# Kernel optimization log

Hardware: AMD Instinct MI355X
Metric: run time of the kernel (lower is better)

The kernel has to match this reference:

```python
import jax, jax.numpy as jnp
import numpy as np

NUM_ATOMS = 100000
NUM_BONDS = 200000
MAX_NB = 6
ATOM_FDIM = 133
BOND_FDIM = 147
HIDDEN = 300
DEPTH = 4
NUM_MOLS = 8192


def setup_inputs() -> dict:
    key = jax.random.key(0)
    ks = jax.random.split(key, 10)
    f_atoms = jax.random.normal(ks[0], (NUM_ATOMS, ATOM_FDIM), dtype=jnp.float32)
    f_bonds = jax.random.normal(ks[1], (NUM_BONDS, BOND_FDIM), dtype=jnp.float32)
    a2b = jax.random.randint(ks[2], (NUM_ATOMS, MAX_NB), 0, NUM_BONDS, dtype=jnp.int32)
    b2a = jax.random.randint(ks[3], (NUM_BONDS,), 0, NUM_ATOMS, dtype=jnp.int32)
    b2revb = jax.random.randint(ks[4], (NUM_BONDS,), 0, NUM_BONDS, dtype=jnp.int32)
    mol_ids = jnp.sort(jax.random.randint(ks[5], (NUM_ATOMS,), 0, NUM_MOLS, dtype=jnp.int32))
    s = 1.0 / np.sqrt(HIDDEN)
    W_i = jax.random.uniform(ks[6], (BOND_FDIM, HIDDEN), jnp.float32, -s, s)
    W_h = jax.random.uniform(ks[7], (HIDDEN, HIDDEN), jnp.float32, -s, s)
    W_o = jax.random.uniform(ks[8], (ATOM_FDIM + HIDDEN, HIDDEN), jnp.float32, -s, s)
    b_o = jax.random.uniform(ks[9], (HIDDEN,), jnp.float32, -s, s)
    return {"f_atoms": f_atoms, "f_bonds": f_bonds, "W_i": W_i, "W_h": W_h,
            "W_o": W_o, "b_o": b_o, "a2b": a2b, "b2a": b2a, "b2revb": b2revb,
            "mol_ids": mol_ids}


def reference(f_atoms, f_bonds, W_i, W_h, W_o, b_o, a2b, b2a, b2revb, mol_ids):
    # initial bond messages: W_i then activation (bias=False)
    inp = f_bonds @ W_i                       # [B, H]
    message = jax.nn.relu(inp)
    for _ in range(DEPTH - 1):
        nei = message[a2b]                    # [A, MAX_NB, H] gather
        a_message = nei.sum(axis=1)           # [A, H]
        rev_message = message[b2revb]         # [B, H]
        message = a_message[b2a] - rev_message
        message = jax.nn.relu(inp + message @ W_h)
    # final atom readout
    a_message = message[a2b].sum(axis=1)      # [A, H]
    a_input = jnp.concatenate([f_atoms, a_message], axis=1)
    atom_hiddens = jax.nn.relu(a_input @ W_o + b_o)
    # per-molecule mean aggregation (== chemprop a_scope loop with 'mean')
    sums = jax.ops.segment_sum(atom_hiddens, mol_ids, num_segments=NUM_MOLS)
    counts = jax.ops.segment_sum(jnp.ones((NUM_ATOMS,), jnp.float32), mol_ids,
                                 num_segments=NUM_MOLS)
    return sums / jnp.maximum(counts, 1.0)[:, None]
```

## Files before the change

### kernel.cpp

```cpp
#include <hip/hip_runtime.h>


#define DEVFN static __device__ __forceinline__

typedef __attribute__((ext_vector_type(8))) __bf16 bf16x8;
typedef __attribute__((ext_vector_type(4))) float floatx4;

DEVFN unsigned short f2bf(float f) {
    unsigned int u = __float_as_uint(f);
    u += 0x7FFFu + ((u >> 16) & 1u);
    return (unsigned short)(u >> 16);
}
DEVFN float bf2f(unsigned int u) { return __uint_as_float(u << 16); }

DEVFN unsigned int bfsub2(unsigned int a, unsigned int m) {
    float lo = bf2f(a & 0xffffu) - bf2f(m & 0xffffu);
    float hi = bf2f(a >> 16) - bf2f(m >> 16);
    return (unsigned int)f2bf(lo) | ((unsigned int)f2bf(hi) << 16);
}
DEVFN uint4 bfsub8(uint4 a, uint4 m) {
    return make_uint4(bfsub2(a.x, m.x), bfsub2(a.y, m.y),
                      bfsub2(a.z, m.z), bfsub2(a.w, m.w));
}

__global__ __launch_bounds__(256) void dbg_fill(float* out, int n, float v) {
    int t = blockIdx.x * 256 + threadIdx.x;
    if (t < n) out[t] = v;
}

__global__ __launch_bounds__(256) void prep_wih(const float* __restrict__ Wi,
                                                const float* __restrict__ Wh,
                                                unsigned short* __restrict__ Wt) {
    int t = blockIdx.x * 256 + threadIdx.x;
    if (t >= 320 * 480) return;
    int n = t / 480, k = t - n * 480;
    float v = 0.f;
    if (n < 300) {
        if (k < 147) v = Wi[k * 300 + n];
        else if (k >= 160 && k < 460) v = Wh[(k - 160) * 300 + n];
    }
    Wt[t] = f2bf(v);
}

__global__ __launch_bounds__(256) void prep_wto(const float* __restrict__ Wo,
                                                unsigned short* __restrict__ Wt) {
    int t = blockIdx.x * 256 + threadIdx.x;
    if (t >= 320 * 448) return;
    int n = t / 448, k = t - n * 448;
    float v = 0.f;
    if (n < 300) {
        if (k < 300) v = Wo[(133 + k) * 300 + n];
        else if (k >= 304 && k < 437) v = Wo[(k - 304) * 300 + n];
    }
    Wt[t] = f2bf(v);
}

__global__ __launch_bounds__(256) void pad_bonds(const float* __restrict__ fb,
                                                 unsigned short* __restrict__ out) {
    int t = blockIdx.x * 256 + threadIdx.x;
    if (t >= 200000 * 20) return;
    int b = t / 20, c = t - b * 20;
    unsigned int o[4];
#pragma unroll
    for (int p = 0; p < 4; ++p) {
        int sc = c * 8 + p * 2;
        float v0 = (sc < 147) ? fb[(size_t)b * 147 + sc] : 0.f;
        float v1 = (sc + 1 < 147) ? fb[(size_t)b * 147 + sc + 1] : 0.f;
        o[p] = (unsigned int)f2bf(v0) | ((unsigned int)f2bf(v1) << 16);
    }
    *(uint4*)(out + (size_t)b * 160 + c * 8) = make_uint4(o[0], o[1], o[2], o[3]);
}

__global__ __launch_bounds__(256) void atoms_concat(const float* __restrict__ fa,
                                                    unsigned short* __restrict__ concat) {
    int t = blockIdx.x * 256 + threadIdx.x;
    if (t >= 100000 * 18) return;
    int a = t / 18, c = t - a * 18;
    unsigned int o[4];
#pragma unroll
    for (int p = 0; p < 4; ++p) {
        int sc = c * 8 + p * 2;
        float v0 = (sc < 133) ? fa[(size_t)a * 133 + sc] : 0.f;
        float v1 = (sc + 1 < 133) ? fa[(size_t)a * 133 + sc + 1] : 0.f;
        o[p] = (unsigned int)f2bf(v0) | ((unsigned int)f2bf(v1) << 16);
    }
    *(uint4*)(concat + (size_t)a * 448 + 304 + c * 8) = make_uint4(o[0], o[1], o[2], o[3]);
}

template <int CH>
__global__ __launch_bounds__(256) void gather_sum(const unsigned short* __restrict__ msg,
                                                  const int* __restrict__ a2b,
                                                  unsigned short* __restrict__ out,
                                                  int ostride, int nA) {
    int t = blockIdx.x * 256 + threadIdx.x;
    if (t >= nA * CH) return;
    int a = t / CH, c = t - a * CH;
    float s[8] = {0, 0, 0, 0, 0, 0, 0, 0};
#pragma unroll
    for (int j = 0; j < 6; ++j) {
        int b = a2b[a * 6 + j];
        uint4 v = *(const uint4*)(msg + (size_t)b * 320 + c * 8);
        s[0] += bf2f(v.x & 0xffffu); s[1] += bf2f(v.x >> 16);
        s[2] += bf2f(v.y & 0xffffu); s[3] += bf2f(v.y >> 16);
        s[4] += bf2f(v.z & 0xffffu); s[5] += bf2f(v.z >> 16);
        s[6] += bf2f(v.w & 0xffffu); s[7] += bf2f(v.w >> 16);
    }
    unsigned int o[4];
#pragma unroll
    for (int p = 0; p < 4; ++p)
        o[p] = (unsigned int)f2bf(s[2 * p]) | ((unsigned int)f2bf(s[2 * p + 1]) << 16);
    *(uint4*)(out + (size_t)a * ostride + c * 8) = make_uint4(o[0], o[1], o[2], o[3]);
}

template <int KT0, int KT1, int MODE, int BSTRIDE>
__global__ __launch_bounds__(256) void gemm_k(const unsigned short* __restrict__ A0,
                                              int a0s,
                                              const unsigned short* __restrict__ amsg,
                                              const unsigned short* __restrict__ msg,
                                              const int* __restrict__ b2a,
                                              const int* __restrict__ b2revb,
                                              const unsigned short* __restrict__ Wt,
                                              unsigned short* __restrict__ outp,
                                              float* __restrict__ hid,
                                              const float* __restrict__ bo, int M) {
    constexpr int KT = KT0 + KT1;
    __shared__ unsigned short As[2 * 5120];
    __shared__ unsigned short Bs[2 * 5120];

    const int tid = threadIdx.x;
    const int lane = tid & 63;
    const int wave = tid >> 6;
    const int wm = wave & 1, wn = wave >> 1;
    const int l16 = lane & 15, quad = lane >> 4;

    int m0, n0;
    {
        const int bid = blockIdx.x;
        const int MB = (int)(gridDim.x >> 1);
        const int mfull = (MB >> 3) << 3;
        const int FULL = mfull << 1;
        int mb, nh;
        if (bid < FULL) {
            nh = (bid >> 3) & 1;
            mb = ((bid >> 4) << 3) + (bid & 7);
        } else {
            const int r = bid - FULL;
            const int rem = MB - mfull;
            nh = (r >= rem) ? 1 : 0;
            mb = mfull + r - nh * rem;
        }
        m0 = mb * 128;
        n0 = nh * 160;
    }

    const int arow = tid >> 1, ahalf = tid & 1;
    const int gr = min(m0 + arow, M - 1);
    const unsigned short* a0p = A0 + (size_t)gr * a0s + ahalf * 16;
    const unsigned short* a1p = nullptr;
    const unsigned short* m1p = nullptr;
    if (KT1 > 0) {
        a1p = amsg + (size_t)b2a[gr] * 320 + ahalf * 16;
        m1p = msg + (size_t)b2revb[gr] * 320 + ahalf * 16;
    }
    const int u0 = tid, u1 = tid + 256, u2 = tid + 512;
    const unsigned short* bg0 = Wt + (size_t)(n0 + (u0 >> 2)) * BSTRIDE + ((u0 ^ (u0 >> 2)) & 3) * 8;
    const unsigned short* bg1 = Wt + (size_t)(n0 + (u1 >> 2)) * BSTRIDE + ((u1 ^ (u1 >> 2)) & 3) * 8;
    const unsigned short* bg2 = (tid < 128)
        ? Wt + (size_t)(n0 + (u2 >> 2)) * BSTRIDE + ((u2 ^ (u2 >> 2)) & 3) * 8 : Wt;

    int aoff[4], boff[5];
#pragma unroll
    for (int tm = 0; tm < 4; ++tm)
        aoff[tm] = (wm * 64 + tm * 16 + l16) * 40 + quad * 8;
#pragma unroll
    for (int tn = 0; tn < 5; ++tn) {
        int nl = wn * 80 + tn * 16 + l16;
        boff[tn] = nl * 32 + ((quad ^ nl) & 3) * 8;
    }

    floatx4 acc[4][5];
#pragma unroll
    for (int tm = 0; tm < 4; ++tm)
#pragma unroll
        for (int tn = 0; tn < 5; ++tn) acc[tm][tn] = (floatx4){0.f, 0.f, 0.f, 0.f};

    uint4 pa0, pa1, pb0, pb1, pb2;
    uint4 qa0, qa1, qb0, qb1, qb2;

    auto ldg = [&](int kt, uint4& x0, uint4& x1, uint4& y0, uint4& y1, uint4& y2) {
        if (kt < KT0) {
            x0 = *(const uint4*)(a0p + kt * 32);
            x1 = *(const uint4*)(a0p + kt * 32 + 8);
        } else {
            int ko = (kt - KT0) * 32;
            uint4 va0 = *(const uint4*)(a1p + ko);
            uint4 va1 = *(const uint4*)(a1p + ko + 8);
            uint4 vm0 = *(const uint4*)(m1p + ko);
            uint4 vm1 = *(const uint4*)(m1p + ko + 8);
            x0 = bfsub8(va0, vm0);
            x1 = bfsub8(va1, vm1);
        }
        y0 = *(const uint4*)(bg0 + kt * 32);
        y1 = *(const uint4*)(bg1 + kt * 32);
        if (tid < 128) y2 = *(const uint4*)(bg2 + kt * 32);
    };
    auto stw = [&](int buf, const uint4& x0, const uint4& x1,
                   const uint4& y0, const uint4& y1, const uint4& y2) {
        unsigned short* ab = As + buf * 5120 + arow * 40 + ahalf * 16;
        *(uint4*)(ab) = x0;
        *(uint4*)(ab + 8) = x1;
        unsigned short* bb = Bs + buf * 5120;
        *(uint4*)(bb + u0 * 8) = y0;
        *(uint4*)(bb + u1 * 8) = y1;
        if (tid < 128) *(uint4*)(bb + u2 * 8) = y2;
    };
    auto barsync = [&]() {
        asm volatile("s_waitcnt lgkmcnt(0)" ::: "memory");
        __builtin_amdgcn_sched_barrier(0);
        __builtin_amdgcn_s_barrier();
        __builtin_amdgcn_sched_barrier(0);
    };
    auto compute = [&](int buf) {
        bf16x8 av[4], bv[5];
#pragma unroll
        for (int tm = 0; tm < 4; ++tm)
            av[tm] = *(const bf16x8*)(As + buf * 5120 + aoff[tm]);
#pragma unroll
        for (int tn = 0; tn < 5; ++tn)
            bv[tn] = *(const bf16x8*)(Bs + buf * 5120 + boff[tn]);
#pragma unroll
        for (int tn = 0; tn < 5; ++tn)
#pragma unroll
            for (int tm = 0; tm < 4; ++tm)
                acc[tm][tn] = __builtin_amdgcn_mfma_f32_16x16x32_bf16(av[tm], bv[tn], acc[tm][tn], 0, 0, 0);
    };

    ldg(0, pa0, pa1, pb0, pb1, pb2);
    if (KT > 1) ldg(1, qa0, qa1, qb0, qb1, qb2);
    stw(0, pa0, pa1, pb0, pb1, pb2);
    barsync();

#pragma unroll
    for (int kt = 0; kt < KT; ++kt) {
        if ((kt & 1) == 0) {
            if (kt + 2 < KT) ldg(kt + 2, pa0, pa1, pb0, pb1, pb2);
            compute(0);
            if (kt + 1 < KT) { stw(1, qa0, qa1, qb0, qb1, qb2); barsync(); }
        } else {
            if (kt + 2 < KT) ldg(kt + 2, qa0, qa1, qb0, qb1, qb2);
            compute(1);
            if (kt + 1 < KT) { stw(0, pa0, pa1, pb0, pb1, pb2); barsync(); }
        }
    }

    float bias[5];
    if (MODE == 2) {
#pragma unroll
        for (int tn = 0; tn < 5; ++tn) {
            int col = n0 + wn * 80 + tn * 16 + l16;
            bias[tn] = (col < 300) ? bo[col] : 0.f;
        }
    }
#pragma unroll
    for (int tm = 0; tm < 4; ++tm) {
        const int r0 = m0 + wm * 64 + tm * 16 + quad * 4;
#pragma unroll
        for (int tn = 0; tn < 5; ++tn) {
            const int col = n0 + wn * 80 + tn * 16 + l16;
#pragma unroll
            for (int i = 0; i < 4; ++i) {
                int r = r0 + i;
                if (r >= M) continue;
                float c = acc[tm][tn][i];
                if (MODE == 2) {
                    if (col < 300) hid[(size_t)r * 300 + col] = fmaxf(c + bias[tn], 0.f);
                } else {
                    outp[(size_t)r * 320 + col] = f2bf(fmaxf(c, 0.f));
                }
            }
        }
    }
}

__global__ __launch_bounds__(320) void mean_k(const float* __restrict__ hid,
                                              const int* __restrict__ mol_ids,
                                              float* __restrict__ out, int nA) {
    int mol = blockIdx.x;
    int lo, hi;
    {
        int l = 0, h = nA;
        while (l < h) { int m = (l + h) >> 1; if (mol_ids[m] < mol) l = m + 1; else h = m; }
        lo = l;
    }
    {
        int l = lo, h = nA;
        while (l < h) { int m = (l + h) >> 1; if (mol_ids[m] < mol + 1) l = m + 1; else h = m; }
        hi = l;
    }
    int col = threadIdx.x;
    if (col >= 300) return;
    float s = 0.f;
    for (int a = lo; a < hi; ++a) s += hid[(size_t)a * 300 + col];
    int cnt = hi - lo;
    out[(size_t)mol * 300 + col] = s / (float)(cnt > 0 ? cnt : 1);
}

extern "C" void kernel_launch(void* const* d_in, const int* in_sizes, int n_in,
                              void* d_out, int out_size, void* d_ws, size_t ws_size,
                              hipStream_t stream) {
    (void)in_sizes; (void)n_in;
    const float* f_atoms = (const float*)d_in[0];
    const float* f_bonds = (const float*)d_in[1];
    const float* W_i     = (const float*)d_in[2];
    const float* W_h     = (const float*)d_in[3];
    const float* W_o     = (const float*)d_in[4];
    const float* b_o     = (const float*)d_in[5];
    const int*   a2b     = (const int*)d_in[6];
    const int*   b2a     = (const int*)d_in[7];
    const int*   b2revb  = (const int*)d_in[8];
    const int*   mol_ids = (const int*)d_in[9];

    const size_t sz_wih  = 320ull * 480 * 2;
    const size_t sz_wto  = 320ull * 448 * 2;
    const size_t sz_fbp  = 200000ull * 160 * 2;
    const size_t sz_amsg = 100000ull * 320 * 2;
    const size_t sz_msg  = 200000ull * 320 * 2;
    const size_t need = sz_wih + sz_wto + sz_fbp + sz_amsg + 2 * sz_msg;

    if (ws_size < need) {
        dbg_fill<<<(out_size + 255) / 256, 256, 0, stream>>>(
            (float*)d_out, out_size, (float)(ws_size >> 20));
        return;
    }

    char* ws = (char*)d_ws;
    unsigned short* wih  = (unsigned short*)(ws);
    unsigned short* wto  = (unsigned short*)(ws + sz_wih);
    unsigned short* fbp  = (unsigned short*)(ws + sz_wih + sz_wto);
    unsigned short* amsg = (unsigned short*)(ws + sz_wih + sz_wto + sz_fbp);
    unsigned short* msgA = (unsigned short*)(ws + sz_wih + sz_wto + sz_fbp + sz_amsg);
    unsigned short* msgB = (unsigned short*)(ws + sz_wih + sz_wto + sz_fbp + sz_amsg + sz_msg);
    unsigned short* concat = msgA;
    float*          hid    = (float*)msgB;

    prep_wih<<<600, 256, 0, stream>>>(W_i, W_h, wih);
    prep_wto<<<560, 256, 0, stream>>>(W_o, wto);
    pad_bonds<<<15625, 256, 0, stream>>>(f_bonds, fbp);

    gemm_k<5, 0, 0, 480><<<dim3(3126), 256, 0, stream>>>(
        fbp, 160, nullptr, nullptr, nullptr, nullptr, wih, msgA, nullptr, nullptr, 200000);

    unsigned short* cur = msgA;
    unsigned short* other = msgB;
    for (int d = 0; d < 3; ++d) {
        gather_sum<40><<<15625, 256, 0, stream>>>(cur, a2b, amsg, 320, 100000);
        gemm_k<5, 10, 0, 480><<<dim3(3126), 256, 0, stream>>>(
            fbp, 160, amsg, cur, b2a, b2revb, wih, other, nullptr, nullptr, 200000);
        unsigned short* t = cur; cur = other; other = t;
    }

    gather_sum<38><<<14844, 256, 0, stream>>>(cur, a2b, concat, 448, 100000);
    atoms_concat<<<7032, 256, 0, stream>>>(f_atoms, concat);
    gemm_k<14, 0, 2, 448><<<dim3(1564), 256, 0, stream>>>(
        concat, 448, nullptr, nullptr, nullptr, nullptr, wto, nullptr, hid, b_o, 100000);
    mean_k<<<8192, 320, 0, stream>>>(hid, mol_ids, (float*)d_out, 100000);
}
```

Baseline: 1.128 ms.

## Pre-pack weights in MFMA fragment order and load B directly into registers

The weight prep kernels now write W in a per-lane MFMA fragment layout (16-column blocks by 32-wide k-tiles), so each wave loads its B operands straight from global memory into registers and skips LDS staging. This removes the B shared-memory buffer, its stores and its LDS reads. In exchange each wave issues more global loads (waves sharing n columns fetch the same data redundantly, relying on cache). The loop is reordered so compute runs before the next prefetch, and launch bounds now request 2 blocks per CU.

Result: no change. 1.138 ms (+0.9%).

```diff
diff --git a/kernel.cpp b/kernel.cpp
--- a/kernel.cpp
+++ b/kernel.cpp
@@ -33,7 +33,12 @@
                                                 unsigned short* __restrict__ Wt) {
     int t = blockIdx.x * 256 + threadIdx.x;
     if (t >= 320 * 480) return;
-    int n = t / 480, k = t - n * 480;
+    int j = t & 7;
+    int lane = (t >> 3) & 63;
+    int rest = t >> 9;
+    int kt = rest % 15, nb = rest / 15;
+    int n = nb * 16 + (lane & 15);
+    int k = kt * 32 + (lane >> 4) * 8 + j;
     float v = 0.f;
     if (n < 300) {
         if (k < 147) v = Wi[k * 300 + n];
@@ -46,7 +51,12 @@
                                                 unsigned short* __restrict__ Wt) {
     int t = blockIdx.x * 256 + threadIdx.x;
     if (t >= 320 * 448) return;
-    int n = t / 448, k = t - n * 448;
+    int j = t & 7;
+    int lane = (t >> 3) & 63;
+    int rest = t >> 9;
+    int kt = rest % 14, nb = rest / 14;
+    int n = nb * 16 + (lane & 15);
+    int k = kt * 32 + (lane >> 4) * 8 + j;
     float v = 0.f;
     if (n < 300) {
         if (k < 300) v = Wo[(133 + k) * 300 + n];
@@ -112,20 +122,19 @@
     *(uint4*)(out + (size_t)a * ostride + c * 8) = make_uint4(o[0], o[1], o[2], o[3]);
 }
 
-template <int KT0, int KT1, int MODE, int BSTRIDE>
-__global__ __launch_bounds__(256) void gemm_k(const unsigned short* __restrict__ A0,
-                                              int a0s,
-                                              const unsigned short* __restrict__ amsg,
-                                              const unsigned short* __restrict__ msg,
-                                              const int* __restrict__ b2a,
-                                              const int* __restrict__ b2revb,
-                                              const unsigned short* __restrict__ Wt,
-                                              unsigned short* __restrict__ outp,
-                                              float* __restrict__ hid,
-                                              const float* __restrict__ bo, int M) {
+template <int KT0, int KT1, int MODE, int WNB>
+__global__ __launch_bounds__(256, 2) void gemm_k(const unsigned short* __restrict__ A0,
+                                                 int a0s,
+                                                 const unsigned short* __restrict__ amsg,
+                                                 const unsigned short* __restrict__ msg,
+                                                 const int* __restrict__ b2a,
+                                                 const int* __restrict__ b2revb,
+                                                 const unsigned short* __restrict__ Wf,
+                                                 unsigned short* __restrict__ outp,
+                                                 float* __restrict__ hid,
+                                                 const float* __restrict__ bo, int M) {
     constexpr int KT = KT0 + KT1;
     __shared__ unsigned short As[2 * 5120];
-    __shared__ unsigned short Bs[2 * 5120];
 
     const int tid = threadIdx.x;
     const int lane = tid & 63;
@@ -162,21 +171,17 @@
         a1p = amsg + (size_t)b2a[gr] * 320 + ahalf * 16;
         m1p = msg + (size_t)b2revb[gr] * 320 + ahalf * 16;
     }
-    const int u0 = tid, u1 = tid + 256, u2 = tid + 512;
-    const unsigned short* bg0 = Wt + (size_t)(n0 + (u0 >> 2)) * BSTRIDE + ((u0 ^ (u0 >> 2)) & 3) * 8;
-    const unsigned short* bg1 = Wt + (size_t)(n0 + (u1 >> 2)) * BSTRIDE + ((u1 ^ (u1 >> 2)) & 3) * 8;
-    const unsigned short* bg2 = (tid < 128)
-        ? Wt + (size_t)(n0 + (u2 >> 2)) * BSTRIDE + ((u2 ^ (u2 >> 2)) & 3) * 8 : Wt;
-
-    int aoff[4], boff[5];
+
+    const int nbase = (n0 >> 4) + wn * 5;
+    const unsigned short* pB[5];
+#pragma unroll
+    for (int tn = 0; tn < 5; ++tn)
+        pB[tn] = Wf + (size_t)(nbase + tn) * (WNB * 512) + lane * 8;
+
+    int aoff[4];
 #pragma unroll
     for (int tm = 0; tm < 4; ++tm)
         aoff[tm] = (wm * 64 + tm * 16 + l16) * 40 + quad * 8;
-#pragma unroll
-    for (int tn = 0; tn < 5; ++tn) {
-        int nl = wn * 80 + tn * 16 + l16;
-        boff[tn] = nl * 32 + ((quad ^ nl) & 3) * 8;
-    }
 
     floatx4 acc[4][5];
 #pragma unroll
@@ -184,35 +189,33 @@
 #pragma unroll
         for (int tn = 0; tn < 5; ++tn) acc[tm][tn] = (floatx4){0.f, 0.f, 0.f, 0.f};
 
-    uint4 pa0, pa1, pb0, pb1, pb2;
-    uint4 qa0, qa1, qb0, qb1, qb2;
-
-    auto ldg = [&](int kt, uint4& x0, uint4& x1, uint4& y0, uint4& y1, uint4& y2) {
+    uint4 aP0, aP1, bP0, bP1, bP2, bP3, bP4;
+    uint4 aQ0, aQ1, bQ0, bQ1, bQ2, bQ3, bQ4;
+
+    auto ldg = [&](int kt, uint4& a0r, uint4& a1r,
+                   uint4& b0, uint4& b1, uint4& b2, uint4& b3, uint4& b4) {
         if (kt < KT0) {
-            x0 = *(const uint4*)(a0p + kt * 32);
-            x1 = *(const uint4*)(a0p + kt * 32 + 8);
+            a0r = *(const uint4*)(a0p + kt * 32);
+            a1r = *(const uint4*)(a0p + kt * 32 + 8);
         } else {
             int ko = (kt - KT0) * 32;
             uint4 va0 = *(const uint4*)(a1p + ko);
             uint4 va1 = *(const uint4*)(a1p + ko + 8);
             uint4 vm0 = *(const uint4*)(m1p + ko);
             uint4 vm1 = *(const uint4*)(m1p + ko + 8);
-            x0 = bfsub8(va0, vm0);
-            x1 = bfsub8(va1, vm1);
-        }
-        y0 = *(const uint4*)(bg0 + kt * 32);
-        y1 = *(const uint4*)(bg1 + kt * 32);
-        if (tid < 128) y2 = *(const uint4*)(bg2 + kt * 32);
+            a0r = bfsub8(va0, vm0);
+            a1r = bfsub8(va1, vm1);
+        }
+        b0 = *(const uint4*)(pB[0] + kt * 512);
+        b1 = *(const uint4*)(pB[1] + kt * 512);
+        b2 = *(const uint4*)(pB[2] + kt * 512);
+        b3 = *(const uint4*)(pB[3] + kt * 512);
+        b4 = *(const uint4*)(pB[4] + kt * 512);
     };
-    auto stw = [&](int buf, const uint4& x0, const uint4& x1,
-                   const uint4& y0, const uint4& y1, const uint4& y2) {
+    auto stw = [&](int buf, const uint4& a0r, const uint4& a1r) {
         unsigned short* ab = As + buf * 5120 + arow * 40 + ahalf * 16;
-        *(uint4*)(ab) = x0;
-        *(uint4*)(ab + 8) = x1;
-        unsigned short* bb = Bs + buf * 5120;
-        *(uint4*)(bb + u0 * 8) = y0;
-        *(uint4*)(bb + u1 * 8) = y1;
-        if (tid < 128) *(uint4*)(bb + u2 * 8) = y2;
+        *(uint4*)(ab) = a0r;
+        *(uint4*)(ab + 8) = a1r;
     };
     auto barsync = [&]() {
         asm volatile("s_waitcnt lgkmcnt(0)" ::: "memory");
@@ -220,14 +223,16 @@
         __builtin_amdgcn_s_barrier();
         __builtin_amdgcn_sched_barrier(0);
     };
-    auto compute = [&](int buf) {
-        bf16x8 av[4], bv[5];
+    auto compute = [&](int buf, const uint4& b0, const uint4& b1,
+                       const uint4& b2, const uint4& b3, const uint4& b4) {
+        bf16x8 av[4];
 #pragma unroll
         for (int tm = 0; tm < 4; ++tm)
             av[tm] = *(const bf16x8*)(As + buf * 5120 + aoff[tm]);
-#pragma unroll
-        for (int tn = 0; tn < 5; ++tn)
-            bv[tn] = *(const bf16x8*)(Bs + buf * 5120 + boff[tn]);
+        const bf16x8 bv[5] = {
+            __builtin_bit_cast(bf16x8, b0), __builtin_bit_cast(bf16x8, b1),
+            __builtin_bit_cast(bf16x8, b2), __builtin_bit_cast(bf16x8, b3),
+            __builtin_bit_cast(bf16x8, b4)};
 #pragma unroll
         for (int tn = 0; tn < 5; ++tn)
 #pragma unroll
@@ -235,21 +240,22 @@
                 acc[tm][tn] = __builtin_amdgcn_mfma_f32_16x16x32_bf16(av[tm], bv[tn], acc[tm][tn], 0, 0, 0);
     };
 
-    ldg(0, pa0, pa1, pb0, pb1, pb2);
-    if (KT > 1) ldg(1, qa0, qa1, qb0, qb1, qb2);
-    stw(0, pa0, pa1, pb0, pb1, pb2);
+    ldg(0, aP0, aP1, bP0, bP1, bP2, bP3, bP4);
+    if (KT > 1) ldg(1, aQ0, aQ1, bQ0, bQ1, bQ2, bQ3, bQ4);
+    stw(0, aP0, aP1);
     barsync();
 
 #pragma unroll
     for (int kt = 0; kt < KT; ++kt) {
+        const int buf = kt & 1;
         if ((kt & 1) == 0) {
-            if (kt + 2 < KT) ldg(kt + 2, pa0, pa1, pb0, pb1, pb2);
-            compute(0);
-            if (kt + 1 < KT) { stw(1, qa0, qa1, qb0, qb1, qb2); barsync(); }
+            compute(buf, bP0, bP1, bP2, bP3, bP4);
+            if (kt + 2 < KT) ldg(kt + 2, aP0, aP1, bP0, bP1, bP2, bP3, bP4);
+            if (kt + 1 < KT) { stw(buf ^ 1, aQ0, aQ1); barsync(); }
         } else {
-            if (kt + 2 < KT) ldg(kt + 2, qa0, qa1, qb0, qb1, qb2);
-            compute(1);
-            if (kt + 1 < KT) { stw(0, pa0, pa1, pb0, pb1, pb2); barsync(); }
+            compute(buf, bQ0, bQ1, bQ2, bQ3, bQ4);
+            if (kt + 2 < KT) ldg(kt + 2, aQ0, aQ1, bQ0, bQ1, bQ2, bQ3, bQ4);
+            if (kt + 1 < KT) { stw(buf ^ 1, aP0, aP1); barsync(); }
         }
     }
 
@@ -347,21 +353,21 @@
     prep_wto<<<560, 256, 0, stream>>>(W_o, wto);
     pad_bonds<<<15625, 256, 0, stream>>>(f_bonds, fbp);
 
-    gemm_k<5, 0, 0, 480><<<dim3(3126), 256, 0, stream>>>(
+    gemm_k<5, 0, 0, 15><<<dim3(3126), 256, 0, stream>>>(
         fbp, 160, nullptr, nullptr, nullptr, nullptr, wih, msgA, nullptr, nullptr, 200000);
 
     unsigned short* cur = msgA;
     unsigned short* other = msgB;
     for (int d = 0; d < 3; ++d) {
         gather_sum<40><<<15625, 256, 0, stream>>>(cur, a2b, amsg, 320, 100000);
-        gemm_k<5, 10, 0, 480><<<dim3(3126), 256, 0, stream>>>(
+        gemm_k<5, 10, 0, 15><<<dim3(3126), 256, 0, stream>>>(
             fbp, 160, amsg, cur, b2a, b2revb, wih, other, nullptr, nullptr, 200000);
         unsigned short* t = cur; cur = other; other = t;
     }
 
     gather_sum<38><<<14844, 256, 0, stream>>>(cur, a2b, concat, 448, 100000);
     atoms_concat<<<7032, 256, 0, stream>>>(f_atoms, concat);
-    gemm_k<14, 0, 2, 448><<<dim3(1564), 256, 0, stream>>>(
+    gemm_k<14, 0, 2, 14><<<dim3(1564), 256, 0, stream>>>(
         concat, 448, nullptr, nullptr, nullptr, nullptr, wto, nullptr, hid, b_o, 100000);
     mean_k<<<8192, 320, 0, stream>>>(hid, mol_ids, (float*)d_out, 100000);
 }
```
